# Kernel optimization log

Measured on AMD Instinct MI355X. Metric: run time of the kernel, lower is better.

## Reference

```python
import jax, jax.numpy as jnp
import numpy as np

B, L, D = 4, 1024, 768
HH = 12            # BERT attention heads
E, M = 30, 60      # entities / mentions per sample
P = E * (E - 1)    # 870 head-tail entity pairs
R = 97             # relation classes
BLK = 64           # block_size
NH = D // BLK      # 12 EGAT heads / bilinear groups
MIN = 1e-10


def setup_inputs():
    key = jax.random.key(0)
    ks = jax.random.split(key, 16)
    context = jax.random.normal(ks[0], (B, L, D), jnp.float32) * 0.1
    attention = jax.random.uniform(ks[1], (B, HH, L, L), jnp.float32)
    attention = attention / attention.sum(-1, keepdims=True)  # row-stochastic like softmax attn
    pos = jax.random.randint(ks[2], (B, M), 0, L)
    mention_map = (jnp.arange(L)[None, None, :] == pos[..., None]).astype(jnp.float32)  # [B,M,L] one-hot
    entity_map = (jnp.arange(M)[None, :] // 2 == jnp.arange(E)[:, None]).astype(jnp.float32)
    entity_map = jnp.broadcast_to(entity_map[None], (B, E, M))  # entity e owns mentions 2e,2e+1
    pairs = np.array([(i, j) for i in range(E) for j in range(E) if i != j], np.int64)
    hts = jnp.broadcast_to(jnp.asarray(pairs)[None], (B, P, 2))
    w = lambda k, s: jax.random.normal(k, s, jnp.float32) * 0.02
    return dict(
        context=context, attention=attention, mention_map=mention_map,
        entity_map=entity_map, hts=hts,
        W_h=w(ks[3], (2 * D, D)), b_h=jnp.zeros((D,), jnp.float32),
        W_t=w(ks[4], (2 * D, D)), b_t=jnp.zeros((D,), jnp.float32),
        W_node=w(ks[5], (D, NH * BLK)),
        W_ni=w(ks[6], (D, NH * BLK)), W_nj=w(ks[7], (D, NH * BLK)),
        W_fij=w(ks[8], (D, NH * BLK)), egat_bias=jnp.zeros((NH * BLK,), jnp.float32),
        attn_vec=w(ks[9], (NH, BLK)),
        W_rel=w(ks[10], (D * BLK, R)), b_rel=jnp.zeros((R,), jnp.float32),
    )


def reference(context, attention, mention_map, entity_map, hts,
              W_h, b_h, W_t, b_t, W_node, W_ni, W_nj, W_fij,
              egat_bias, attn_vec, W_rel, b_rel):
    bidx = jnp.arange(B)[:, None]
    ht_mask = (hts.sum(-1) != 0)[..., None].astype(context.dtype)  # [B,P,1]

    # ---- log-sum-exp entity pooling over mentions (get_ht) ----
    mention = jnp.exp(jnp.einsum('bml,bld->bmd', mention_map, context))  # [B,M,D]
    ent = jnp.einsum('bem,bmd->bed', entity_map, mention)                # [B,E,D]
    empty = entity_map.sum(-1, keepdims=True) == 0
    entity = jnp.log(jnp.where(empty, 1.0, ent))                          # [B,E,D]

    # ---- attention-weighted context pooling ----
    em = jnp.einsum('bem,bml->bel', entity_map, mention_map)             # entity -> token map
    em = em / (em.sum(-1, keepdims=True) + MIN)
    ea = jnp.einsum('bel,bhlm->behm', em, attention)                     # [B,E,HH,L]
    ah = ea[bidx, hts[..., 0]]                                            # [B,P,HH,L]
    at = ea[bidx, hts[..., 1]]
    ca = (ah * at).sum(2)                                                 # [B,P,L]
    ca = ca / (ca.sum(-1, keepdims=True) + MIN)
    context_info = jnp.einsum('bpl,bld->bpd', ca, context) * ht_mask      # [B,P,D]

    # ---- batched graph: all hts pairs are edges, plus self loops ----
    N = B * E
    off = (jnp.arange(B) * E)[:, None]
    src = jnp.concatenate([(hts[..., 0] + off).reshape(-1), jnp.arange(N)])
    dst = jnp.concatenate([(hts[..., 1] + off).reshape(-1), jnp.arange(N)])
    x = entity.reshape(N, D)
    efeat = jnp.concatenate([context_info.reshape(B * P, D), x], axis=0)  # pair edges then self loops

    # ---- EGATConv ----
    f_ni = (x @ W_ni).reshape(N, NH, BLK)
    f_nj = (x @ W_nj).reshape(N, NH, BLK)
    f_fij = (efeat @ W_fij).reshape(-1, NH, BLK)
    f_out = f_ni[src] + f_nj[dst] + f_fij + egat_bias.reshape(NH, BLK)    # [Etot,NH,BLK]
    e = jax.nn.leaky_relu(f_out, 0.2)
    scores = (e * attn_vec[None]).sum(-1)                                  # [Etot,NH]
    smax = jax.ops.segment_max(scores, dst, num_segments=N)
    ex = jnp.exp(scores - smax[dst])
    ssum = jax.ops.segment_sum(ex, dst, num_segments=N)
    alpha = ex / ssum[dst]                                                 # edge softmax over in-edges
    msg = (x @ W_node).reshape(N, NH, BLK)[src] * alpha[..., None]
    nodes = jax.ops.segment_sum(msg, dst, num_segments=N)                  # [N,NH,BLK]

    edge_ctx = f_out[:B * P].reshape(B, P, D)                              # get_res (all edges kept, order preserved)
    node_feat = nodes.reshape(B, E, D)

    # ---- get_new_ht + dense + tanh ----
    new_h = jnp.tanh(jnp.concatenate([node_feat[bidx, hts[..., 0]], edge_ctx], -1) @ W_h + b_h)
    new_t = jnp.tanh(jnp.concatenate([node_feat[bidx, hts[..., 1]], edge_ctx], -1) @ W_t + b_t)

    # ---- group biLinear relation classifier ----
    a = new_h.reshape(B, P, NH, BLK)
    b = new_t.reshape(B, P, NH, BLK)
    bl = jnp.einsum('bpkx,bpky->bpkxy', a, b).reshape(B, P, NH * BLK * BLK)
    return bl @ W_rel + b_rel                                              # [B,P,R]
```

## Files before the change

### kernel.cpp

```cpp
#include <hip/hip_runtime.h>
#include <math.h>

#define BB 4
#define LLL 1024
#define DDD 768
#define HHH 12
#define EEE 30
#define MMM 60
#define PPP 870
#define RRR 97
#define NNODE 120
#define NPAIR 3480
#define NEDGE 3600
#define FMIN 1e-10f

typedef __attribute__((ext_vector_type(8))) __bf16 bf16x8;
typedef __attribute__((ext_vector_type(8))) short short8;
typedef __attribute__((ext_vector_type(8))) _Float16 f16x8;
typedef __attribute__((ext_vector_type(4))) float f32x4;
typedef __attribute__((ext_vector_type(4))) unsigned short u16x4;

static __device__ __forceinline__ unsigned short f2bf(float v) {
  return __builtin_bit_cast(unsigned short, (__bf16)v);
}
static __device__ __forceinline__ unsigned short f2h(float v) {
  return __builtin_bit_cast(unsigned short, (_Float16)v);
}
static __device__ __forceinline__ float bf2f(unsigned short u) {
  unsigned int x = ((unsigned int)u) << 16;
  return __builtin_bit_cast(float, x);
}

__global__ __launch_bounds__(256) void k_entity(const float* __restrict__ ctx,
                                                const float* __restrict__ mmap,
                                                const float* __restrict__ emap,
                                                unsigned short* __restrict__ xb) {
  int be = blockIdx.x;
  int b = be / EEE;
  int tid = threadIdx.x;
  __shared__ int s_cnt;
  __shared__ int s_l[16];
  __shared__ float s_w[16];
  float acc[3] = {0.f, 0.f, 0.f};
  float csum = 0.f;
  for (int m = 0; m < MMM; m++) {
    float wm = emap[(size_t)be * MMM + m];
    csum += wm;
    if (wm == 0.f) continue;
    if (tid == 0) s_cnt = 0;
    __syncthreads();
    const float* mrow = mmap + ((size_t)b * MMM + m) * LLL;
    #pragma unroll
    for (int q = 0; q < 4; q++) {
      int l = tid + 256 * q;
      float w = mrow[l];
      if (w != 0.f) {
        int i = atomicAdd(&s_cnt, 1);
        if (i < 16) { s_l[i] = l; s_w[i] = w; }
      }
    }
    __syncthreads();
    int c = min(s_cnt, 16);
    float dot[3] = {0.f, 0.f, 0.f};
    for (int i = 0; i < c; i++) {
      const float* cr = ctx + ((size_t)b * LLL + s_l[i]) * DDD;
      float w = s_w[i];
      #pragma unroll
      for (int q = 0; q < 3; q++) dot[q] += w * cr[tid + 256 * q];
    }
    #pragma unroll
    for (int q = 0; q < 3; q++) acc[q] += wm * expf(dot[q]);
  }
  bool empty = (csum == 0.f);
  #pragma unroll
  for (int q = 0; q < 3; q++)
    xb[(size_t)be * DDD + tid + 256 * q] = f2bf(empty ? 0.f : logf(acc[q]));
}

__global__ __launch_bounds__(256) void k_em(const float* __restrict__ emap,
                                            const float* __restrict__ mmap,
                                            int* __restrict__ nzl,
                                            float* __restrict__ nzw,
                                            int* __restrict__ nzc) {
  int be = blockIdx.x;
  int b = be / EEE;
  int tid = threadIdx.x;
  __shared__ float em_s[1024];
  __shared__ float red[256];
  float acc[4] = {0.f, 0.f, 0.f, 0.f};
  for (int m = 0; m < MMM; m++) {
    float w = emap[(size_t)be * MMM + m];
    if (w != 0.f) {
      const float* mr = mmap + ((size_t)b * MMM + m) * LLL;
      #pragma unroll
      for (int q = 0; q < 4; q++) acc[q] += w * mr[tid + 256 * q];
    }
  }
  red[tid] = acc[0] + acc[1] + acc[2] + acc[3];
  __syncthreads();
  for (int st = 128; st > 0; st >>= 1) {
    if (tid < st) red[tid] += red[tid + st];
    __syncthreads();
  }
  float inv = 1.f / (red[0] + FMIN);
  #pragma unroll
  for (int q = 0; q < 4; q++) em_s[tid + 256 * q] = acc[q] * inv;
  __syncthreads();
  if (tid < 64) {
    int base = 0;
    for (int l0 = 0; l0 < LLL; l0 += 64) {
      float w = em_s[l0 + tid];
      unsigned long long mb = __ballot(w != 0.f);
      int pre = __popcll(mb & ((1ull << tid) - 1ull));
      if (w != 0.f) {
        nzl[be * LLL + base + pre] = l0 + tid;
        nzw[be * LLL + base + pre] = w;
      }
      base += __popcll(mb);
    }
    if (tid == 0) nzc[be] = base;
  }
}

__global__ __launch_bounds__(256) void k_ea(const float* __restrict__ attn,
                                            const int* __restrict__ nzl,
                                            const float* __restrict__ nzw,
                                            const int* __restrict__ nzc,
                                            unsigned short* __restrict__ ea) {
  int e = blockIdx.x, h = blockIdx.y, b = blockIdx.z;
  int be = b * EEE + e;
  int cnt = nzc[be];
  float acc[4] = {0.f, 0.f, 0.f, 0.f};
  for (int i = 0; i < cnt; i++) {
    int l = nzl[be * LLL + i];
    float w = nzw[be * LLL + i];
    const float* ar = attn + (((size_t)b * HHH + h) * LLL + l) * LLL;
    #pragma unroll
    for (int q = 0; q < 4; q++) acc[q] += w * ar[threadIdx.x + 256 * q];
  }
  unsigned short* er = ea + ((size_t)be * HHH + h) * LLL;
  #pragma unroll
  for (int q = 0; q < 4; q++) er[threadIdx.x + 256 * q] = f2bf(acc[q]);
}

__global__ __launch_bounds__(256) void k_ca(const unsigned short* __restrict__ ea,
                                            const int* __restrict__ hts,
                                            unsigned short* __restrict__ cab) {
  int bp = blockIdx.x;
  int b = bp / PPP;
  int hs = hts[bp * 2 + 0], ts = hts[bp * 2 + 1];
  int tid = threadIdx.x;
  const unsigned short* eh = ea + (size_t)(b * EEE + hs) * HHH * LLL;
  const unsigned short* et = ea + (size_t)(b * EEE + ts) * HHH * LLL;
  float v[4] = {0.f, 0.f, 0.f, 0.f};
  #pragma unroll
  for (int h = 0; h < HHH; h++) {
    u16x4 hv = *(const u16x4*)&eh[h * LLL + tid * 4];
    u16x4 tv = *(const u16x4*)&et[h * LLL + tid * 4];
    #pragma unroll
    for (int q = 0; q < 4; q++) v[q] += bf2f(hv[q]) * bf2f(tv[q]);
  }
  __shared__ float red[256];
  red[tid] = v[0] + v[1] + v[2] + v[3];
  __syncthreads();
  for (int st = 128; st > 0; st >>= 1) {
    if (tid < st) red[tid] += red[tid + st];
    __syncthreads();
  }
  float inv = 1.f / (red[0] + FMIN);
  u16x4 o;
  #pragma unroll
  for (int q = 0; q < 4; q++) o[q] = f2bf(v[q] * inv);
  *(u16x4*)&cab[(size_t)bp * LLL + tid * 4] = o;
}

__global__ __launch_bounds__(256) void k_transpose(const float* __restrict__ src,
                                                   unsigned short* __restrict__ dst,
                                                   int R, int C) {
  __shared__ float t_s[32][33];
  int c0 = blockIdx.x * 32, r0 = blockIdx.y * 32;
  const float* s = src + (size_t)blockIdx.z * R * C;
  unsigned short* d = dst + (size_t)blockIdx.z * R * C;
  int tx = threadIdx.x & 31, ty = threadIdx.x >> 5;
  #pragma unroll
  for (int i = 0; i < 4; i++)
    t_s[ty + i * 8][tx] = s[(size_t)(r0 + ty + i * 8) * C + c0 + tx];
  __syncthreads();
  #pragma unroll
  for (int i = 0; i < 4; i++)
    d[(size_t)(c0 + ty + i * 8) * R + r0 + tx] = f2bf(t_s[tx][ty + i * 8]);
}

struct TWArgs { const float* src[6]; unsigned short* dst[6]; };
__global__ __launch_bounds__(256) void k_transpose_w(TWArgs a) {
  int z = blockIdx.z;
  int R = (z < 4) ? DDD : 2 * DDD;
  int r0 = blockIdx.y * 32;
  if (r0 >= R) return;
  int c0 = blockIdx.x * 32;
  __shared__ float t_s[32][33];
  const float* s = a.src[z];
  unsigned short* d = a.dst[z];
  int tx = threadIdx.x & 31, ty = threadIdx.x >> 5;
  #pragma unroll
  for (int i = 0; i < 4; i++)
    t_s[ty + i * 8][tx] = s[(size_t)(r0 + ty + i * 8) * DDD + c0 + tx];
  __syncthreads();
  #pragma unroll
  for (int i = 0; i < 4; i++)
    d[(size_t)(c0 + ty + i * 8) * R + r0 + tx] = f2bf(t_s[tx][ty + i * 8]);
}

struct MGArgs {
  const unsigned short *A, *A2, *BT0, *BT1, *BT2, *nodes;
  float *C0, *C1, *C2;
  unsigned short *Cb;
  unsigned short *Ch, *Ct;
  const float *bias0, *bias1;
  const float *fni, *fnj, *ebias, *avec;
  float *scores;
  const int *hts;
  int M, K;
};

template <int MODE>
__global__ __launch_bounds__(256) void k_mgemm(MGArgs g) {
  __shared__ unsigned short As[3][64 * 64];
  __shared__ unsigned short Bs[3][64 * 64];
  int tid = threadIdx.x;
  int lane = tid & 63;
  int wv = tid >> 6;
  int l15 = lane & 15, l4 = lane >> 4;
  int wr = wv >> 1, wc = wv & 1;
  int row0 = blockIdx.x * 64, col0 = blockIdx.y * 64;
  int bz = blockIdx.z;
  int K = g.K;

  const unsigned short* BTp;
  if (MODE == 0) BTp = g.BT0 + (size_t)bz * DDD * LLL;
  else if (MODE == 1) BTp = bz == 0 ? g.BT0 : (bz == 1 ? g.BT1 : g.BT2);
  else if (MODE == 2) BTp = g.BT0;
  else BTp = bz ? g.BT1 : g.BT0;

  int sgg = (lane & 7) ^ ((lane >> 3) & 7);
  int srsub = lane >> 3;

  const unsigned short* gaA[2];
  const unsigned short* gaA2[2];
  const unsigned short* gaB[2];
  #pragma unroll
  for (int jj = 0; jj < 2; jj++) {
    int j = wv * 2 + jj;
    int row = j * 8 + srsub;
    int grow = row0 + row; if (grow >= g.M) grow = g.M - 1;
    if (MODE == 0) {
      gaA[jj] = g.A + ((size_t)(bz * PPP) + grow) * LLL + sgg * 8;
    } else if (MODE == 1) {
      gaA[jj] = g.A + (size_t)grow * DDD + sgg * 8;
    } else if (MODE == 2) {
      gaA[jj] = (grow < NPAIR) ? g.A + (size_t)grow * DDD + sgg * 8
                               : g.A2 + (size_t)(grow - NPAIR) * DDD + sgg * 8;
    } else {
      int b = grow / PPP;
      int node = b * EEE + g.hts[grow * 2 + bz];
      gaA[jj] = g.nodes + (size_t)node * DDD + sgg * 8;
      gaA2[jj] = g.A2 + (size_t)grow * DDD + sgg * 8;
    }
    gaB[jj] = BTp + (size_t)(col0 + row) * K + sgg * 8;
  }

  auto stage = [&](int buf, int t) {
    int k = t * 64;
    #pragma unroll
    for (int jj = 0; jj < 2; jj++) {
      int j = wv * 2 + jj;
      const unsigned short* ga;
      if (MODE == 3) ga = (k < DDD) ? gaA[jj] + k : gaA2[jj] + (k - DDD);
      else ga = gaA[jj] + k;
      const unsigned short* gb = gaB[jj] + k;
      __builtin_amdgcn_global_load_lds(
          (const __attribute__((address_space(1))) unsigned int*)ga,
          (__attribute__((address_space(3))) unsigned int*)&As[buf][j * 512],
          16, 0, 0);
      __builtin_amdgcn_global_load_lds(
          (const __attribute__((address_space(1))) unsigned int*)gb,
          (__attribute__((address_space(3))) unsigned int*)&Bs[buf][j * 512],
          16, 0, 0);
    }
  };

  f32x4 zero = {0.f, 0.f, 0.f, 0.f};
  f32x4 acc[2][2];
  #pragma unroll
  for (int m = 0; m < 2; m++)
    #pragma unroll
    for (int n = 0; n < 2; n++) acc[m][n] = zero;

  int nt = K / 64;
  stage(0, 0);
  stage(1, 1);
  asm volatile("s_waitcnt vmcnt(4)" ::: "memory");
  __builtin_amdgcn_s_barrier();

  int cur = 0;
  for (int t = 0; t < nt; t++) {
    if (t + 2 < nt) {
      int nxt2 = cur - 1; if (nxt2 < 0) nxt2 = 2;
      stage(nxt2, t + 2);
    }
    short8 af[2][2], bfr[2][2];
    #pragma unroll
    for (int ks = 0; ks < 2; ks++) {
      #pragma unroll
      for (int m = 0; m < 2; m++) {
        int row = wr * 32 + m * 16 + l15;
        int phys = (ks * 4 + l4) ^ (row & 7);
        af[ks][m] = *(const short8*)&As[cur][row * 64 + phys * 8];
      }
      #pragma unroll
      for (int n = 0; n < 2; n++) {
        int row = wc * 32 + n * 16 + l15;
        int phys = (ks * 4 + l4) ^ (row & 7);
        bfr[ks][n] = *(const short8*)&Bs[cur][row * 64 + phys * 8];
      }
    }
    #pragma unroll
    for (int ks = 0; ks < 2; ks++)
      #pragma unroll
      for (int m = 0; m < 2; m++)
        #pragma unroll
        for (int n = 0; n < 2; n++)
          acc[m][n] = __builtin_amdgcn_mfma_f32_16x16x32_bf16(af[ks][m], bfr[ks][n], acc[m][n], 0, 0, 0);
    if (t + 1 < nt) {
      if (t + 2 < nt) asm volatile("s_waitcnt vmcnt(4)" ::: "memory");
      else            asm volatile("s_waitcnt vmcnt(0)" ::: "memory");
      __builtin_amdgcn_s_barrier();
    }
    cur += 1; if (cur == 3) cur = 0;
  }

  float* score_s = (float*)&As[0][0];
  if (MODE == 2) {
    if (tid < 64) score_s[tid] = 0.f;
    __syncthreads();
  }

  #pragma unroll
  for (int m = 0; m < 2; m++) {
    int rbase = row0 + wr * 32 + m * 16 + l4 * 4;
    #pragma unroll
    for (int n = 0; n < 2; n++) {
      int col = col0 + wc * 32 + n * 16 + l15;
      #pragma unroll
      for (int q = 0; q < 4; q++) {
        int r = rbase + q;
        if (r >= g.M) continue;
        float v = acc[m][n][q];
        if (MODE == 0) {
          size_t grow = (size_t)bz * PPP + r;
          int h0 = g.hts[grow * 2 + 0], h1 = g.hts[grow * 2 + 1];
          float mk = (h0 + h1 != 0) ? 1.f : 0.f;
          g.Cb[grow * DDD + col] = f2bf(v * mk);
        } else if (MODE == 1) {
          float* C = bz == 0 ? g.C0 : (bz == 1 ? g.C1 : g.C2);
          C[(size_t)r * DDD + col] = v;
        } else if (MODE == 2) {
          int srcn, dstn;
          if (r < NPAIR) {
            int bb = r / PPP;
            srcn = bb * EEE + g.hts[r * 2 + 0];
            dstn = bb * EEE + g.hts[r * 2 + 1];
          } else {
            srcn = dstn = r - NPAIR;
          }
          float vv = v + g.fni[(size_t)srcn * DDD + col] +
                     g.fnj[(size_t)dstn * DDD + col] + g.ebias[col];
          g.Cb[(size_t)r * DDD + col] = f2bf(vv);
          float lrv = vv > 0.f ? vv : 0.2f * vv;
          atomicAdd(&score_s[r - row0], lrv * g.avec[col]);
        } else {
          unsigned short* C = bz ? g.Ct : g.Ch;
          const float* bias = bz ? g.bias1 : g.bias0;
          C[(size_t)r * DDD + col] = f2h(tanhf(v + bias[col]));
        }
      }
    }
  }

  if (MODE == 2) {
    __syncthreads();
    if (tid < 64) {
      int r = row0 + tid;
      if (r < g.M) g.scores[r * HHH + blockIdx.y] = score_s[tid];
    }
  }
}

#define ECAP 256
__global__ __launch_bounds__(256) void k_agg(const float* __restrict__ scores,
                                             const float* __restrict__ fnode,
                                             const int* __restrict__ hts,
                                             unsigned short* __restrict__ nodesb) {
  __shared__ int cnt;
  __shared__ int elist[ECAP], slist[ECAP];
  __shared__ float smax[HHH], ssum[HHH];
  __shared__ float alpha[ECAP * HHH];
  int n = blockIdx.x, tid = threadIdx.x;
  if (tid == 0) cnt = 0;
  __syncthreads();
  for (int e = tid; e < NEDGE; e += 256) {
    int srcn, dstn;
    if (e < NPAIR) {
      int b = e / PPP;
      srcn = b * EEE + hts[e * 2 + 0];
      dstn = b * EEE + hts[e * 2 + 1];
    } else {
      srcn = dstn = e - NPAIR;
    }
    if (dstn == n) {
      int i = atomicAdd(&cnt, 1);
      if (i < ECAP) { elist[i] = e; slist[i] = srcn; }
    }
  }
  __syncthreads();
  int c = min(cnt, ECAP);
  if (tid < HHH) {
    float m = -1e30f;
    for (int i = 0; i < c; i++) m = fmaxf(m, scores[elist[i] * HHH + tid]);
    smax[tid] = m;
    float s = 0.f;
    for (int i = 0; i < c; i++) s += expf(scores[elist[i] * HHH + tid] - m);
    ssum[tid] = s;
  }
  __syncthreads();
  for (int t = tid; t < c * HHH; t += 256) {
    int i = t / HHH, h = t - i * HHH;
    alpha[t] = expf(scores[elist[i] * HHH + h] - smax[h]) / ssum[h];
  }
  __syncthreads();
  for (int j = tid; j < DDD; j += 256) {
    int h = j >> 6;
    float acc = 0.f;
    for (int i = 0; i < c; i++)
      acc += alpha[i * HHH + h] * fnode[(size_t)slist[i] * DDD + j];
    nodesb[(size_t)n * DDD + j] = f2bf(acc);
  }
}

__global__ __launch_bounds__(256) void k_initout(const float* __restrict__ brel,
                                                 float* __restrict__ out) {
  int idx = blockIdx.x * 256 + threadIdx.x;
  if (idx < NPAIR * RRR) out[idx] = brel[idx % RRR];
}

__global__ __launch_bounds__(256) void k_wprep(const float* __restrict__ Wrel,
                                               unsigned short* __restrict__ tW) {
  __shared__ float w_s[64][98];
  int c = blockIdx.x;
  int tid = threadIdx.x;
  for (int idx = tid; idx < 64 * 97; idx += 256) {
    int y = idx / 97, r = idx - y * 97;
    w_s[y][r] = Wrel[(size_t)(c * 64 + y) * RRR + r];
  }
  __syncthreads();
  for (int odx = tid; odx < 8192; odx += 256) {
    int nt = odx >> 10, h = (odx >> 9) & 1, lane = (odx >> 3) & 63, i = odx & 7;
    int y = 32 * h + 8 * (lane >> 4) + i;
    int r = nt * 16 + (lane & 15);
    float v = (r < RRR) ? w_s[y][r] : 0.f;
    tW[(size_t)c * 8192 + odx] = f2h(v);
  }
}

__global__ __launch_bounds__(256) void k_bilinear_mfma(
    const unsigned short* __restrict__ newh, const unsigned short* __restrict__ newt,
    const unsigned short* __restrict__ tW, float* __restrict__ out) {
  __shared__ unsigned short a_s[64][64];
  int tid = threadIdx.x;
  int lane = tid & 63;
  int wv = tid >> 6;
  int l15 = lane & 15, l4 = lane >> 4;
  int bid = blockIdx.x;
  int kg = bid / 55, pt = bid - kg * 55;

  {
    int pl = tid >> 2, xq = (tid & 3) * 16;
    int prow = pt * 64 + pl; if (prow >= NPAIR) prow = NPAIR - 1;
    const unsigned short* src = newh + (size_t)prow * DDD + kg * 64 + xq;
    #pragma unroll
    for (int half16 = 0; half16 < 2; half16++) {
      u16x4 v0 = *(const u16x4*)(src + half16 * 8);
      u16x4 v1 = *(const u16x4*)(src + half16 * 8 + 4);
      #pragma unroll
      for (int i = 0; i < 4; i++) {
        a_s[xq + half16 * 8 + i][pl] = v0[i];
        a_s[xq + half16 * 8 + 4 + i][pl] = v1[i];
      }
    }
  }

  f16x8 bfrag[4][2];
  #pragma unroll
  for (int t = 0; t < 4; t++) {
    int prow = pt * 64 + t * 16 + l15; if (prow >= NPAIR) prow = NPAIR - 1;
    const unsigned short* src = newt + (size_t)prow * DDD + kg * 64 + 8 * l4;
    #pragma unroll
    for (int h = 0; h < 2; h++)
      bfrag[t][h] = __builtin_bit_cast(f16x8, *(const uint4*)(src + h * 32));
  }
  __syncthreads();

  f32x4 zero = {0.f, 0.f, 0.f, 0.f};
  f32x4 acc[4][2];
  #pragma unroll
  for (int t = 0; t < 4; t++) { acc[t][0] = zero; acc[t][1] = zero; }

  const unsigned short* wp = tW + (size_t)(kg * 64) * 8192 + lane * 8;
  int o00 = (wv * 2 + 0) << 9;
  int o01 = (wv * 2 + 1) << 9;
  int o10 = ((wv + 4) * 2 + 0) << 9;
  int o11 = ((wv + 4) * 2 + 1) << 9;

  auto loadw = [&](uint4* wf, int x) {
    const unsigned short* p = wp + (size_t)x * 8192;
    wf[0] = *(const uint4*)(p + o00);
    wf[1] = *(const uint4*)(p + o01);
    wf[2] = *(const uint4*)(p + o10);
    wf[3] = *(const uint4*)(p + o11);
  };
  auto step = [&](const uint4* wf, int x) {
    f16x8 a8[4];
    #pragma unroll
    for (int t = 0; t < 4; t++) {
      unsigned int av = a_s[x][t * 16 + l15];
      unsigned int aw = (av << 16) | av;
      uint4 ab = {aw, aw, aw, aw};
      a8[t] = __builtin_bit_cast(f16x8, ab);
    }
    #pragma unroll
    for (int h = 0; h < 2; h++) {
      f16x8 w0 = __builtin_bit_cast(f16x8, wf[h]);
      f16x8 w1 = __builtin_bit_cast(f16x8, wf[2 + h]);
      #pragma unroll
      for (int t = 0; t < 4; t++) {
        f16x8 gv = a8[t] * bfrag[t][h];
        acc[t][0] = __builtin_amdgcn_mfma_f32_16x16x32_f16(gv, w0, acc[t][0], 0, 0, 0);
        acc[t][1] = __builtin_amdgcn_mfma_f32_16x16x32_f16(gv, w1, acc[t][1], 0, 0, 0);
      }
    }
  };

  uint4 wa[4], wb[4];
  loadw(wa, 0);
  for (int xx = 0; xx < 64; xx += 2) {
    loadw(wb, xx + 1);
    step(wa, xx);
    if (xx + 2 < 64) loadw(wa, xx + 2);
    step(wb, xx + 1);
  }

  #pragma unroll
  for (int n = 0; n < 2; n++) {
    int r = (wv + 4 * n) * 16 + l15;
    if (r >= RRR) continue;
    #pragma unroll
    for (int t = 0; t < 4; t++) {
      int pbase = pt * 64 + t * 16 + l4 * 4;
      #pragma unroll
      for (int q = 0; q < 4; q++) {
        int p = pbase + q;
        if (p < NPAIR) atomicAdd(&out[(size_t)p * RRR + r], acc[t][n][q]);
      }
    }
  }
}

extern "C" void kernel_launch(void* const* d_in, const int* in_sizes, int n_in,
                              void* d_out, int out_size, void* d_ws, size_t ws_size,
                              hipStream_t stream) {
  const float* context   = (const float*)d_in[0];
  const float* attention = (const float*)d_in[1];
  const float* mmap      = (const float*)d_in[2];
  const float* emap      = (const float*)d_in[3];
  const int*   hts       = (const int*)d_in[4];
  const float* W_h       = (const float*)d_in[5];
  const float* b_h       = (const float*)d_in[6];
  const float* W_t       = (const float*)d_in[7];
  const float* b_t       = (const float*)d_in[8];
  const float* W_node    = (const float*)d_in[9];
  const float* W_ni      = (const float*)d_in[10];
  const float* W_nj      = (const float*)d_in[11];
  const float* W_fij     = (const float*)d_in[12];
  const float* egat_bias = (const float*)d_in[13];
  const float* attn_vec  = (const float*)d_in[14];
  const float* W_rel     = (const float*)d_in[15];
  const float* b_rel     = (const float*)d_in[16];
  float* out = (float*)d_out;

  float* ws = (float*)d_ws;
  size_t o = 0;
  auto alloc = [&](size_t n) { size_t r = o; o += (n + 63) & ~(size_t)63; return r; };
  auto halloc = [&](size_t nshorts) { return alloc((nshorts + 1) / 2); };
  size_t o_xb      = halloc((size_t)NNODE * DDD);
  size_t o_ea      = halloc((size_t)BB * EEE * HHH * LLL);
  size_t o_cab     = halloc((size_t)NPAIR * LLL);
  size_t o_ctxT    = halloc((size_t)BB * DDD * LLL);
  size_t o_wtni    = halloc((size_t)DDD * DDD);
  size_t o_wtnj    = halloc((size_t)DDD * DDD);
  size_t o_wtnode  = halloc((size_t)DDD * DDD);
  size_t o_wtfij   = halloc((size_t)DDD * DDD);
  size_t o_wth     = halloc((size_t)DDD * 2 * DDD);
  size_t o_wtt     = halloc((size_t)DDD * 2 * DDD);
  size_t o_cinfob  = halloc((size_t)NPAIR * DDD);
  size_t o_fni     = alloc((size_t)NNODE * DDD);
  size_t o_fnj     = alloc((size_t)NNODE * DDD);
  size_t o_fnode   = alloc((size_t)NNODE * DDD);
  size_t o_foutb   = halloc((size_t)NEDGE * DDD);
  size_t o_scores  = alloc((size_t)NEDGE * HHH);
  size_t o_nodesb  = halloc((size_t)NNODE * DDD);
  size_t o_newh    = halloc((size_t)NPAIR * DDD);
  size_t o_newt    = halloc((size_t)NPAIR * DDD);
  size_t o_nzl     = alloc((size_t)BB * EEE * LLL);
  size_t o_nzw     = alloc((size_t)BB * EEE * LLL);
  size_t o_nzc     = alloc(128);
  size_t o_tw      = halloc((size_t)768 * 8192);
  (void)ws_size;

  unsigned short* xb     = (unsigned short*)(ws + o_xb);
  unsigned short* ea     = (unsigned short*)(ws + o_ea);
  unsigned short* cab    = (unsigned short*)(ws + o_cab);
  unsigned short* ctxT   = (unsigned short*)(ws + o_ctxT);
  unsigned short* wtni   = (unsigned short*)(ws + o_wtni);
  unsigned short* wtnj   = (unsigned short*)(ws + o_wtnj);
  unsigned short* wtnode = (unsigned short*)(ws + o_wtnode);
  unsigned short* wtfij  = (unsigned short*)(ws + o_wtfij);
  unsigned short* wth    = (unsigned short*)(ws + o_wth);
  unsigned short* wtt    = (unsigned short*)(ws + o_wtt);
  unsigned short* cinfob = (unsigned short*)(ws + o_cinfob);
  float* fni     = ws + o_fni;
  float* fnj     = ws + o_fnj;
  float* fnode   = ws + o_fnode;
  unsigned short* foutb  = (unsigned short*)(ws + o_foutb);
  float* scores  = ws + o_scores;
  unsigned short* nodesb = (unsigned short*)(ws + o_nodesb);
  unsigned short* newh   = (unsigned short*)(ws + o_newh);
  unsigned short* newt   = (unsigned short*)(ws + o_newt);
  int*   nzl     = (int*)(ws + o_nzl);
  float* nzw     = ws + o_nzw;
  int*   nzc     = (int*)(ws + o_nzc);
  unsigned short* tW = (unsigned short*)(ws + o_tw);

  k_wprep<<<768, 256, 0, stream>>>(W_rel, tW);
  k_transpose<<<dim3(24, 32, BB), 256, 0, stream>>>(context, ctxT, LLL, DDD);
  TWArgs ta;
  ta.src[0] = W_ni;  ta.dst[0] = wtni;
  ta.src[1] = W_nj;  ta.dst[1] = wtnj;
  ta.src[2] = W_node; ta.dst[2] = wtnode;
  ta.src[3] = W_fij; ta.dst[3] = wtfij;
  ta.src[4] = W_h;   ta.dst[4] = wth;
  ta.src[5] = W_t;   ta.dst[5] = wtt;
  k_transpose_w<<<dim3(24, 48, 6), 256, 0, stream>>>(ta);

  k_entity<<<BB * EEE, 256, 0, stream>>>(context, mmap, emap, xb);
  k_em<<<BB * EEE, 256, 0, stream>>>(emap, mmap, nzl, nzw, nzc);
  k_ea<<<dim3(EEE, HHH, BB), 256, 0, stream>>>(attention, nzl, nzw, nzc, ea);
  k_ca<<<BB * PPP, 256, 0, stream>>>(ea, hts, cab);

  MGArgs gc = {};
  gc.A = cab; gc.BT0 = ctxT; gc.Cb = cinfob; gc.hts = hts; gc.M = PPP; gc.K = LLL;
  k_mgemm<0><<<dim3(14, 12, BB), 256, 0, stream>>>(gc);

  MGArgs gf = {};
  gf.A = xb; gf.BT0 = wtni; gf.BT1 = wtnj; gf.BT2 = wtnode;
  gf.C0 = fni; gf.C1 = fnj; gf.C2 = fnode; gf.M = NNODE; gf.K = DDD;
  k_mgemm<1><<<dim3(2, 12, 3), 256, 0, stream>>>(gf);

  MGArgs gj = {};
  gj.A = cinfob; gj.A2 = xb; gj.BT0 = wtfij; gj.Cb = foutb;
  gj.fni = fni; gj.fnj = fnj; gj.ebias = egat_bias; gj.avec = attn_vec;
  gj.scores = scores; gj.hts = hts; gj.M = NEDGE; gj.K = DDD;
  k_mgemm<2><<<dim3(57, 12, 1), 256, 0, stream>>>(gj);

  k_agg<<<NNODE, 256, 0, stream>>>(scores, fnode, hts, nodesb);

  MGArgs gn = {};
  gn.A2 = foutb; gn.nodes = nodesb; gn.BT0 = wth; gn.BT1 = wtt;
  gn.bias0 = b_h; gn.bias1 = b_t; gn.Ch = newh; gn.Ct = newt;
  gn.hts = hts; gn.M = NPAIR; gn.K = 2 * DDD;
  k_mgemm<3><<<dim3(55, 12, 2), 256, 0, stream>>>(gn);

  k_initout<<<(NPAIR * RRR + 255) / 256, 256, 0, stream>>>(b_rel, out);
  k_bilinear_mfma<<<55 * 12, 256, 0, stream>>>(newh, newt, tW, out);
}
```

Baseline: 243.2 us.

## Merge independent prep kernels into one launch and skip padded MFMA tiles

Five independent preprocessing kernels (W_rel repack, context transpose, weight transposes, entity pooling, entity-mention nonzero extraction) are combined into a single launch that dispatches on block index. Output bias initialisation moves into the k_ca kernel, removing another launch. In the bilinear MFMA kernel, waves whose second relation tile lies entirely past R=97 skip those weight loads and MFMAs. This cuts launch overhead and wasted padded compute, at the cost of a larger, heterogeneous prep kernel whose shared-memory footprint is the union of all bodies, which can reduce occupancy.

```diff
diff --git a/kernel.cpp b/kernel.cpp
--- a/kernel.cpp
+++ b/kernel.cpp
@@ -31,16 +31,62 @@
   return __builtin_bit_cast(float, x);
 }
 
-__global__ __launch_bounds__(256) void k_entity(const float* __restrict__ ctx,
-                                                const float* __restrict__ mmap,
-                                                const float* __restrict__ emap,
-                                                unsigned short* __restrict__ xb) {
-  int be = blockIdx.x;
-  int b = be / EEE;
+struct PrepArgs {
+  const float *Wrel, *context, *mmap, *emap;
+  const float *wsrc[6];
+  unsigned short *tW, *ctxT, *xb;
+  unsigned short *wdst[6];
+  int *nzl, *nzc;
+  float *nzw;
+};
+
+#define NB_WPREP 768
+#define NB_CTX   (24 * 32 * BB)
+#define NB_WT    (24 * 48 * 6)
+#define NB_ENT   NNODE
+#define NB_EM    NNODE
+
+static __device__ void body_wprep(int c, const float* __restrict__ Wrel,
+                                  unsigned short* __restrict__ tW) {
+  __shared__ float w_s[64][98];
   int tid = threadIdx.x;
+  for (int idx = tid; idx < 64 * 97; idx += 256) {
+    int y = idx / 97, r = idx - y * 97;
+    w_s[y][r] = Wrel[(size_t)(c * 64 + y) * RRR + r];
+  }
+  __syncthreads();
+  for (int odx = tid; odx < 8192; odx += 256) {
+    int nt = odx >> 10, h = (odx >> 9) & 1, lane = (odx >> 3) & 63, i = odx & 7;
+    int y = 32 * h + 8 * (lane >> 4) + i;
+    int r = nt * 16 + (lane & 15);
+    float v = (r < RRR) ? w_s[y][r] : 0.f;
+    tW[(size_t)c * 8192 + odx] = f2h(v);
+  }
+}
+
+static __device__ void body_transpose(int bx, int by, const float* __restrict__ s,
+                                      unsigned short* __restrict__ d, int R, int C) {
+  __shared__ float t_s[32][33];
+  int c0 = bx * 32, r0 = by * 32;
+  int tx = threadIdx.x & 31, ty = threadIdx.x >> 5;
+  #pragma unroll
+  for (int i = 0; i < 4; i++)
+    t_s[ty + i * 8][tx] = s[(size_t)(r0 + ty + i * 8) * C + c0 + tx];
+  __syncthreads();
+  #pragma unroll
+  for (int i = 0; i < 4; i++)
+    d[(size_t)(c0 + ty + i * 8) * R + r0 + tx] = f2bf(t_s[tx][ty + i * 8]);
+}
+
+static __device__ void body_entity(int be, const float* __restrict__ ctx,
+                                   const float* __restrict__ mmap,
+                                   const float* __restrict__ emap,
+                                   unsigned short* __restrict__ xb) {
   __shared__ int s_cnt;
   __shared__ int s_l[16];
   __shared__ float s_w[16];
+  int b = be / EEE;
+  int tid = threadIdx.x;
   float acc[3] = {0.f, 0.f, 0.f};
   float csum = 0.f;
   for (int m = 0; m < MMM; m++) {
@@ -77,16 +123,14 @@
     xb[(size_t)be * DDD + tid + 256 * q] = f2bf(empty ? 0.f : logf(acc[q]));
 }
 
-__global__ __launch_bounds__(256) void k_em(const float* __restrict__ emap,
-                                            const float* __restrict__ mmap,
-                                            int* __restrict__ nzl,
-                                            float* __restrict__ nzw,
-                                            int* __restrict__ nzc) {
-  int be = blockIdx.x;
+static __device__ void body_em(int be, const float* __restrict__ emap,
+                               const float* __restrict__ mmap,
+                               int* __restrict__ nzl, float* __restrict__ nzw,
+                               int* __restrict__ nzc) {
+  __shared__ float em_s[1024];
+  __shared__ float red[256];
   int b = be / EEE;
   int tid = threadIdx.x;
-  __shared__ float em_s[1024];
-  __shared__ float red[256];
   float acc[4] = {0.f, 0.f, 0.f, 0.f};
   for (int m = 0; m < MMM; m++) {
     float w = emap[(size_t)be * MMM + m];
@@ -120,6 +164,35 @@
     }
     if (tid == 0) nzc[be] = base;
   }
+}
+
+__global__ __launch_bounds__(256) void k_prep(PrepArgs a) {
+  int bid = blockIdx.x;
+  if (bid < NB_WPREP) {
+    body_wprep(bid, a.Wrel, a.tW);
+    return;
+  }
+  bid -= NB_WPREP;
+  if (bid < NB_CTX) {
+    int bx = bid % 24, by = (bid / 24) % 32, bz = bid / (24 * 32);
+    body_transpose(bx, by, a.context + (size_t)bz * LLL * DDD,
+                   a.ctxT + (size_t)bz * DDD * LLL, LLL, DDD);
+    return;
+  }
+  bid -= NB_CTX;
+  if (bid < NB_WT) {
+    int bx = bid % 24, by = (bid / 24) % 48, bz = bid / (24 * 48);
+    int R = (bz < 4) ? DDD : 2 * DDD;
+    if (by * 32 < R) body_transpose(bx, by, a.wsrc[bz], a.wdst[bz], R, DDD);
+    return;
+  }
+  bid -= NB_WT;
+  if (bid < NB_ENT) {
+    body_entity(bid, a.context, a.mmap, a.emap, a.xb);
+    return;
+  }
+  bid -= NB_ENT;
+  body_em(bid, a.emap, a.mmap, a.nzl, a.nzw, a.nzc);
 }
 
 __global__ __launch_bounds__(256) void k_ea(const float* __restrict__ attn,
@@ -145,11 +218,14 @@
 
 __global__ __launch_bounds__(256) void k_ca(const unsigned short* __restrict__ ea,
                                             const int* __restrict__ hts,
-                                            unsigned short* __restrict__ cab) {
+                                            unsigned short* __restrict__ cab,
+                                            const float* __restrict__ brel,
+                                            float* __restrict__ out) {
   int bp = blockIdx.x;
   int b = bp / PPP;
   int hs = hts[bp * 2 + 0], ts = hts[bp * 2 + 1];
   int tid = threadIdx.x;
+  if (tid < RRR) out[(size_t)bp * RRR + tid] = brel[tid];
   const unsigned short* eh = ea + (size_t)(b * EEE + hs) * HHH * LLL;
   const unsigned short* et = ea + (size_t)(b * EEE + ts) * HHH * LLL;
   float v[4] = {0.f, 0.f, 0.f, 0.f};
@@ -172,43 +248,6 @@
   #pragma unroll
   for (int q = 0; q < 4; q++) o[q] = f2bf(v[q] * inv);
   *(u16x4*)&cab[(size_t)bp * LLL + tid * 4] = o;
-}
-
-__global__ __launch_bounds__(256) void k_transpose(const float* __restrict__ src,
-                                                   unsigned short* __restrict__ dst,
-                                                   int R, int C) {
-  __shared__ float t_s[32][33];
-  int c0 = blockIdx.x * 32, r0 = blockIdx.y * 32;
-  const float* s = src + (size_t)blockIdx.z * R * C;
-  unsigned short* d = dst + (size_t)blockIdx.z * R * C;
-  int tx = threadIdx.x & 31, ty = threadIdx.x >> 5;
-  #pragma unroll
-  for (int i = 0; i < 4; i++)
-    t_s[ty + i * 8][tx] = s[(size_t)(r0 + ty + i * 8) * C + c0 + tx];
-  __syncthreads();
-  #pragma unroll
-  for (int i = 0; i < 4; i++)
-    d[(size_t)(c0 + ty + i * 8) * R + r0 + tx] = f2bf(t_s[tx][ty + i * 8]);
-}
-
-struct TWArgs { const float* src[6]; unsigned short* dst[6]; };
-__global__ __launch_bounds__(256) void k_transpose_w(TWArgs a) {
-  int z = blockIdx.z;
-  int R = (z < 4) ? DDD : 2 * DDD;
-  int r0 = blockIdx.y * 32;
-  if (r0 >= R) return;
-  int c0 = blockIdx.x * 32;
-  __shared__ float t_s[32][33];
-  const float* s = a.src[z];
-  unsigned short* d = a.dst[z];
-  int tx = threadIdx.x & 31, ty = threadIdx.x >> 5;
-  #pragma unroll
-  for (int i = 0; i < 4; i++)
-    t_s[ty + i * 8][tx] = s[(size_t)(r0 + ty + i * 8) * DDD + c0 + tx];
-  __syncthreads();
-  #pragma unroll
-  for (int i = 0; i < 4; i++)
-    d[(size_t)(c0 + ty + i * 8) * R + r0 + tx] = f2bf(t_s[tx][ty + i * 8]);
 }
 
 struct MGArgs {
@@ -447,31 +486,6 @@
   }
 }
 
-__global__ __launch_bounds__(256) void k_initout(const float* __restrict__ brel,
-                                                 float* __restrict__ out) {
-  int idx = blockIdx.x * 256 + threadIdx.x;
-  if (idx < NPAIR * RRR) out[idx] = brel[idx % RRR];
-}
-
-__global__ __launch_bounds__(256) void k_wprep(const float* __restrict__ Wrel,
-                                               unsigned short* __restrict__ tW) {
-  __shared__ float w_s[64][98];
-  int c = blockIdx.x;
-  int tid = threadIdx.x;
-  for (int idx = tid; idx < 64 * 97; idx += 256) {
-    int y = idx / 97, r = idx - y * 97;
-    w_s[y][r] = Wrel[(size_t)(c * 64 + y) * RRR + r];
-  }
-  __syncthreads();
-  for (int odx = tid; odx < 8192; odx += 256) {
-    int nt = odx >> 10, h = (odx >> 9) & 1, lane = (odx >> 3) & 63, i = odx & 7;
-    int y = 32 * h + 8 * (lane >> 4) + i;
-    int r = nt * 16 + (lane & 15);
-    float v = (r < RRR) ? w_s[y][r] : 0.f;
-    tW[(size_t)c * 8192 + odx] = f2h(v);
-  }
-}
-
 __global__ __launch_bounds__(256) void k_bilinear_mfma(
     const unsigned short* __restrict__ newh, const unsigned short* __restrict__ newt,
     const unsigned short* __restrict__ tW, float* __restrict__ out) {
@@ -482,6 +496,7 @@
   int l15 = lane & 15, l4 = lane >> 4;
   int bid = blockIdx.x;
   int kg = bid / 55, pt = bid - kg * 55;
+  bool use1 = ((wv + 4) * 16) < RRR;
 
   {
     int pl = tid >> 2, xq = (tid & 3) * 16;
@@ -525,8 +540,10 @@
     const unsigned short* p = wp + (size_t)x * 8192;
     wf[0] = *(const uint4*)(p + o00);
     wf[1] = *(const uint4*)(p + o01);
-    wf[2] = *(const uint4*)(p + o10);
-    wf[3] = *(const uint4*)(p + o11);
+    if (use1) {
+      wf[2] = *(const uint4*)(p + o10);
+      wf[3] = *(const uint4*)(p + o11);
+    }
   };
   auto step = [&](const uint4* wf, int x) {
     f16x8 a8[4];
@@ -545,7 +562,8 @@
       for (int t = 0; t < 4; t++) {
         f16x8 gv = a8[t] * bfrag[t][h];
         acc[t][0] = __builtin_amdgcn_mfma_f32_16x16x32_f16(gv, w0, acc[t][0], 0, 0, 0);
-        acc[t][1] = __builtin_amdgcn_mfma_f32_16x16x32_f16(gv, w1, acc[t][1], 0, 0, 0);
+        if (use1)
+          acc[t][1] = __builtin_amdgcn_mfma_f32_16x16x32_f16(gv, w1, acc[t][1], 0, 0, 0);
       }
     }
   };
@@ -650,21 +668,20 @@
   int*   nzc     = (int*)(ws + o_nzc);
   unsigned short* tW = (unsigned short*)(ws + o_tw);
 
-  k_wprep<<<768, 256, 0, stream>>>(W_rel, tW);
-  k_transpose<<<dim3(24, 32, BB), 256, 0, stream>>>(context, ctxT, LLL, DDD);
-  TWArgs ta;
-  ta.src[0] = W_ni;  ta.dst[0] = wtni;
-  ta.src[1] = W_nj;  ta.dst[1] = wtnj;
-  ta.src[2] = W_node; ta.dst[2] = wtnode;
-  ta.src[3] = W_fij; ta.dst[3] = wtfij;
-  ta.src[4] = W_h;   ta.dst[4] = wth;
-  ta.src[5] = W_t;   ta.dst[5] = wtt;
-  k_transpose_w<<<dim3(24, 48, 6), 256, 0, stream>>>(ta);
-
-  k_entity<<<BB * EEE, 256, 0, stream>>>(context, mmap, emap, xb);
-  k_em<<<BB * EEE, 256, 0, stream>>>(emap, mmap, nzl, nzw, nzc);
+  PrepArgs pa;
+  pa.Wrel = W_rel; pa.context = context; pa.mmap = mmap; pa.emap = emap;
+  pa.wsrc[0] = W_ni;  pa.wdst[0] = wtni;
+  pa.wsrc[1] = W_nj;  pa.wdst[1] = wtnj;
+  pa.wsrc[2] = W_node; pa.wdst[2] = wtnode;
+  pa.wsrc[3] = W_fij; pa.wdst[3] = wtfij;
+  pa.wsrc[4] = W_h;   pa.wdst[4] = wth;
+  pa.wsrc[5] = W_t;   pa.wdst[5] = wtt;
+  pa.tW = tW; pa.ctxT = ctxT; pa.xb = xb;
+  pa.nzl = nzl; pa.nzw = nzw; pa.nzc = nzc;
+  k_prep<<<NB_WPREP + NB_CTX + NB_WT + NB_ENT + NB_EM, 256, 0, stream>>>(pa);
+
   k_ea<<<dim3(EEE, HHH, BB), 256, 0, stream>>>(attention, nzl, nzw, nzc, ea);
-  k_ca<<<BB * PPP, 256, 0, stream>>>(ea, hts, cab);
+  k_ca<<<BB * PPP, 256, 0, stream>>>(ea, hts, cab, b_rel, out);
 
   MGArgs gc = {};
   gc.A = cab; gc.BT0 = ctxT; gc.Cb = cinfob; gc.hts = hts; gc.M = PPP; gc.K = LLL;
@@ -689,6 +706,5 @@
   gn.hts = hts; gn.M = NPAIR; gn.K = 2 * DDD;
   k_mgemm<3><<<dim3(55, 12, 2), 256, 0, stream>>>(gn);
 
-  k_initout<<<(NPAIR * RRR + 255) / 256, 256, 0, stream>>>(b_rel, out);
   k_bilinear_mfma<<<55 * 12, 256, 0, stream>>>(newh, newt, tW, out);
 }
```

Result: faster. 227.1 us (-6.6%).
